# Kernel tuning notes

Hardware: AMD Instinct MI355X
Metric: run time of the kernel (lower is better)

Reference implementation:

```python
import jax, jax.numpy as jnp
import numpy as np

# Model hyperparameters (from init_kwargs)
D_MODEL, D_STATE, D_CONV, EXPAND, NHEADS, NGROUPS = 1024, 16, 4, 2, 8, 1
D_INNER = D_MODEL * EXPAND                      # 2048
HEADDIM = D_INNER // NHEADS                     # 256
D_XBC = D_INNER + 2 * NGROUPS * D_STATE         # conv channels: x + B + C
D_IN_PROJ = 3 * D_INNER + D_XBC + NHEADS        # z0 + x0 + z(unused) + xBC + dt
BATCH, SEQLEN = 2, 2048
LN_EPS = 1e-5


def setup_inputs() -> dict:
    key = jax.random.key(0)
    ks = jax.random.split(key, 8)
    u = jax.random.normal(ks[0], (BATCH, SEQLEN, D_MODEL), dtype=jnp.float32)
    W_in = jax.random.normal(ks[1], (D_IN_PROJ, D_MODEL), jnp.float32) / np.sqrt(D_MODEL)
    conv_w = jax.random.normal(ks[2], (D_XBC, 1, D_CONV), jnp.float32) / np.sqrt(D_CONV)
    conv_b = jnp.zeros((D_XBC,), jnp.float32)
    # dt_bias = inverse-softplus of dt ~ LogUniform(1e-3, 1e-1), as in source init
    dt = jnp.exp(jax.random.uniform(ks[3], (NHEADS,)) * (np.log(0.1) - np.log(0.001)) + np.log(0.001))
    dt_bias = dt + jnp.log(-jnp.expm1(-dt))
    A_log = jnp.log(jax.random.uniform(ks[4], (NHEADS,), minval=0.9, maxval=0.999))
    D_param = jnp.ones((NHEADS,), jnp.float32)
    ln_gamma = jnp.ones((D_INNER,), jnp.float32)
    ln_beta = jnp.zeros((D_INNER,), jnp.float32)
    W_gate = jax.random.normal(ks[5], (D_INNER, D_INNER), jnp.float32) / np.sqrt(D_INNER)
    b_gate = jnp.zeros((D_INNER,), jnp.float32)
    W_out = jax.random.normal(ks[6], (D_MODEL, 2 * D_INNER), jnp.float32) / np.sqrt(2 * D_INNER)
    return dict(u=u, W_in=W_in, conv_w=conv_w, conv_b=conv_b, dt_bias=dt_bias,
                A_log=A_log, D_param=D_param, ln_gamma=ln_gamma, ln_beta=ln_beta,
                W_gate=W_gate, b_gate=b_gate, W_out=W_out)


def _silu(x):
    return x * jax.nn.sigmoid(x)


def reference(u, W_in, conv_w, conv_b, dt_bias, A_log, D_param,
              ln_gamma, ln_beta, W_gate, b_gate, W_out):
    B, L, _ = u.shape
    zxbcdt = u @ W_in.T                                   # [B,L,D_IN_PROJ]
    z0 = zxbcdt[..., :D_INNER]
    x0 = zxbcdt[..., D_INNER:2 * D_INNER]
    # z = zxbcdt[..., 2*D_INNER:3*D_INNER]  # split but never used in source forward
    xBC = zxbcdt[..., 3 * D_INNER:3 * D_INNER + D_XBC]
    dt = jax.nn.softplus(zxbcdt[..., -NHEADS:] + dt_bias)  # [B,L,H]
    A = -jnp.exp(A_log)                                    # [H], per-head scalar

    # causal depthwise conv1d over time (left pad d_conv-1, crop to L)
    xBC_c = jnp.transpose(xBC, (0, 2, 1))                  # [B,C,L]
    xBC_c = jax.lax.conv_general_dilated(
        xBC_c, conv_w, window_strides=(1,), padding=[(D_CONV - 1, 0)],
        dimension_numbers=('NCH', 'OIH', 'NCH'), feature_group_count=D_XBC)
    xBC = _silu(jnp.transpose(xBC_c, (0, 2, 1)) + conv_b)  # [B,L,C]

    x = xBC[..., :D_INNER].reshape(B, L, NHEADS, HEADDIM)  # [B,L,H,P]
    Bm = xBC[..., D_INNER:D_INNER + D_STATE]               # [B,L,N] (ngroups=1)
    Cm = xBC[..., D_INNER + D_STATE:]                      # [B,L,N]

    def step(h, inp):
        x_t, B_t, C_t, dt_t = inp                          # [B,H,P],[B,N],[B,N],[B,H]
        dA = jnp.exp(dt_t * A)[:, :, None, None]           # [B,H,1,1]
        h = dA * h + (dt_t[:, :, None, None] * x_t[..., None]) * B_t[:, None, None, :]
        y_t = jnp.einsum('bhpn,bn->bhp', h, C_t) + D_param[None, :, None] * x_t
        return h, y_t

    h0 = jnp.zeros((B, NHEADS, HEADDIM, D_STATE), u.dtype)
    xs = (jnp.moveaxis(x, 1, 0), jnp.moveaxis(Bm, 1, 0),
          jnp.moveaxis(Cm, 1, 0), jnp.moveaxis(dt, 1, 0))
    _, y = jax.lax.scan(step, h0, xs)                      # [L,B,H,P]
    y = jnp.moveaxis(y, 0, 1).reshape(B, L, D_INNER)

    # LayerNorm
    mu = y.mean(-1, keepdims=True)
    var = ((y - mu) ** 2).mean(-1, keepdims=True)
    y = (y - mu) * jax.lax.rsqrt(var + LN_EPS) * ln_gamma + ln_beta

    gate = jax.nn.sigmoid(y @ W_gate.T + b_gate)
    y = gate * y

    mlp_skip = _silu(z0) * x0
    return jnp.concatenate([mlp_skip, y], axis=-1) @ W_out.T  # [B,L,D_MODEL]
```

## Files before the change

kernel.cpp:

```cpp
#include <hip/hip_runtime.h>
#include <hip/hip_bf16.h>
#include <math.h>

#define BATCH   2
#define SEQLEN  2048
#define DMODEL  1024
#define DINNER  2048
#define DSTATE  16
#define NHEADS  8
#define HEADDIM 256
#define DXBC    2080
#define NPACK   6184
#define NPAD    6400
#define MROWS   4096
#define CHUNK   64
#define NCHUNK  32
#define BH      16

typedef unsigned int u32;
typedef unsigned short u16;
typedef __attribute__((ext_vector_type(8))) short short8;
typedef __attribute__((ext_vector_type(4))) float f32x4;

#define GLOAD16(g, l) __builtin_amdgcn_global_load_lds( \
    (const __attribute__((address_space(1))) u32*)(g),  \
    (__attribute__((address_space(3))) u32*)(l), 16, 0, 0)

#define MFMA_B16(d, a, b) d = __builtin_amdgcn_mfma_f32_16x16x32_bf16(a, b, d, 0, 0, 0)

__device__ __forceinline__ u16 f2bf(float f) {
  union { float f; u32 u; } v; v.f = f;
  u32 r = v.u + 0x7fff + ((v.u >> 16) & 1);
  return (u16)(r >> 16);
}
__device__ __forceinline__ float bf2f(u16 b) {
  union { u32 u; float f; } v; v.u = ((u32)b) << 16;
  return v.f;
}

struct GParts { float* p0; float* p1; };

#define S_U   1048576
#define S_WG  1048576
#define S_WO  1048576
#define S_WP  1638400
#define S_TOT (S_U + S_WG + S_WO + S_WP)

__global__ void cvt_all(const float* __restrict__ u, const float* __restrict__ Wg,
                        const float* __restrict__ Wo, const float* __restrict__ Win,
                        u16* __restrict__ ub, u16* __restrict__ Wgb,
                        u16* __restrict__ Wob, u16* __restrict__ Wp) {
  for (int i = blockIdx.x * 256 + threadIdx.x; i < S_TOT; i += gridDim.x * 256) {
    const float* src; u16* dst; int idx;
    if (i < S_U) { src = u; dst = ub; idx = i; }
    else if (i < S_U + S_WG) { src = Wg; dst = Wgb; idx = i - S_U; }
    else if (i < S_U + S_WG + S_WO) { src = Wo; dst = Wob; idx = i - S_U - S_WG; }
    else {
      int j = i - S_U - S_WG - S_WO;
      int row = j >> 8, c4 = j & 255;
      ushort4 o = make_ushort4(0, 0, 0, 0);
      if (row < NPACK) {
        int orig = row < 4096 ? row : row + 2048;
        float4 v = ((const float4*)(Win + (size_t)orig * DMODEL))[c4];
        o = make_ushort4(f2bf(v.x), f2bf(v.y), f2bf(v.z), f2bf(v.w));
      }
      ((ushort4*)Wp)[j] = o;
      continue;
    }
    float4 v = ((const float4*)src)[idx];
    ((ushort4*)dst)[idx] = make_ushort4(f2bf(v.x), f2bf(v.y), f2bf(v.z), f2bf(v.w));
  }
}

template <int NL>
__device__ __forceinline__ void stage_rows(const u16* __restrict__ gsrc, int ldk,
                                           char* ldsmat, int row0, int w, int l) {
  const int rl = w * 8 + (l >> 3);
  const int q = ((l & 7) ^ (l >> 3)) * 8;
  #pragma unroll
  for (int j = 0; j < NL; ++j) {
    GLOAD16(gsrc + (size_t)(row0 + j * 64 + rl) * ldk + q,
            ldsmat + (row0 + j * 64 + w * 8) * 128);
  }
}

__device__ __forceinline__ short8 frag8(const char* mat, int row, int q) {
  return *(const short8*)(mat + row * 128 + ((q ^ (row & 7)) << 4));
}

__global__ __launch_bounds__(512, 1) void gemmA(
    const u16* __restrict__ A, const u16* __restrict__ B, int K, int ldk,
    int ldo, u16* __restrict__ outp) {
  __shared__ char lds[131072];
  const int tid = threadIdx.x;
  const int w = tid >> 6, l = tid & 63;
  const int wm = w >> 2, wn = w & 3;
  const int fr = l & 15, g = l >> 4;
  int s = blockIdx.y * gridDim.x + blockIdx.x;
  const int nwg = gridDim.x * gridDim.y;
  s = (s & 7) * (nwg >> 3) + (s >> 3);
  const int bx = s % gridDim.x, by = s / gridDim.x;
  const u16* Ap = A + (size_t)bx * 256 * ldk;
  const u16* Bp = B + (size_t)by * 256 * ldk;
  const int NT = K >> 6;

  f32x4 acc[8][4];
  #pragma unroll
  for (int m = 0; m < 8; ++m)
    #pragma unroll
    for (int n = 0; n < 4; ++n) acc[m][n] = (f32x4){0.f, 0.f, 0.f, 0.f};

  stage_rows<2>(Bp, ldk, lds + 32768, 0, w, l);
  stage_rows<2>(Bp, ldk, lds + 32768, 128, w, l);
  stage_rows<1>(Ap, ldk, lds, 0, w, l);
  stage_rows<1>(Ap, ldk, lds, 128, w, l);
  stage_rows<1>(Ap, ldk, lds, 64, w, l);
  stage_rows<1>(Ap, ldk, lds, 192, w, l);

  for (int t = 0; t < NT; ++t) {
    const bool last = (t == NT - 1);
    const char* cbA = lds + (t & 1) * 65536;
    const char* cbB = cbA + 32768;
    char* nbA = lds + ((t + 1) & 1) * 65536;
    char* nbB = nbA + 32768;
    const u16* An = Ap + (size_t)(t + 1) * 64;
    const u16* Bn = Bp + (size_t)(t + 1) * 64;

    asm volatile("s_waitcnt vmcnt(2)" ::: "memory");
    __builtin_amdgcn_s_barrier();
    __builtin_amdgcn_sched_barrier(0);

    short8 bf0[4], bf1[4];
    #pragma unroll
    for (int n = 0; n < 4; ++n) {
      bf0[n] = frag8(cbB, wn * 64 + n * 16 + fr, g);
      bf1[n] = frag8(cbB, wn * 64 + n * 16 + fr, 4 + g);
    }
    {
      short8 a00 = frag8(cbA, wm * 128 + fr, g);
      short8 a01 = frag8(cbA, wm * 128 + fr, 4 + g);
      short8 a10 = frag8(cbA, wm * 128 + 16 + fr, g);
      short8 a11 = frag8(cbA, wm * 128 + 16 + fr, 4 + g);
      if (!last) stage_rows<2>(Bn, ldk, nbB, 0, w, l);
      __builtin_amdgcn_sched_barrier(0);
      __builtin_amdgcn_s_setprio(1);
      #pragma unroll
      for (int n = 0; n < 4; ++n) { MFMA_B16(acc[0][n], a00, bf0[n]); MFMA_B16(acc[1][n], a10, bf0[n]); }
      #pragma unroll
      for (int n = 0; n < 4; ++n) { MFMA_B16(acc[0][n], a01, bf1[n]); MFMA_B16(acc[1][n], a11, bf1[n]); }
      __builtin_amdgcn_s_setprio(0);
    }
    {
      short8 a00 = frag8(cbA, wm * 128 + 32 + fr, g);
      short8 a01 = frag8(cbA, wm * 128 + 32 + fr, 4 + g);
      short8 a10 = frag8(cbA, wm * 128 + 48 + fr, g);
      short8 a11 = frag8(cbA, wm * 128 + 48 + fr, 4 + g);
      if (!last) stage_rows<2>(Bn, ldk, nbB, 128, w, l);
      __builtin_amdgcn_sched_barrier(0);
      __builtin_amdgcn_s_setprio(1);
      #pragma unroll
      for (int n = 0; n < 4; ++n) { MFMA_B16(acc[2][n], a00, bf0[n]); MFMA_B16(acc[3][n], a10, bf0[n]); }
      #pragma unroll
      for (int n = 0; n < 4; ++n) { MFMA_B16(acc[2][n], a01, bf1[n]); MFMA_B16(acc[3][n], a11, bf1[n]); }
      __builtin_amdgcn_s_setprio(0);
    }
    if (last) { asm volatile("s_waitcnt vmcnt(0)" ::: "memory"); }
    else      { asm volatile("s_waitcnt vmcnt(4)" ::: "memory"); }
    __builtin_amdgcn_s_barrier();
    __builtin_amdgcn_sched_barrier(0);
    {
      short8 a00 = frag8(cbA, wm * 128 + 64 + fr, g);
      short8 a01 = frag8(cbA, wm * 128 + 64 + fr, 4 + g);
      short8 a10 = frag8(cbA, wm * 128 + 80 + fr, g);
      short8 a11 = frag8(cbA, wm * 128 + 80 + fr, 4 + g);
      if (!last) { stage_rows<1>(An, ldk, nbA, 0, w, l); stage_rows<1>(An, ldk, nbA, 128, w, l); }
      __builtin_amdgcn_sched_barrier(0);
      __builtin_amdgcn_s_setprio(1);
      #pragma unroll
      for (int n = 0; n < 4; ++n) { MFMA_B16(acc[4][n], a00, bf0[n]); MFMA_B16(acc[5][n], a10, bf0[n]); }
      #pragma unroll
      for (int n = 0; n < 4; ++n) { MFMA_B16(acc[4][n], a01, bf1[n]); MFMA_B16(acc[5][n], a11, bf1[n]); }
      __builtin_amdgcn_s_setprio(0);
    }
    {
      short8 a00 = frag8(cbA, wm * 128 + 96 + fr, g);
      short8 a01 = frag8(cbA, wm * 128 + 96 + fr, 4 + g);
      short8 a10 = frag8(cbA, wm * 128 + 112 + fr, g);
      short8 a11 = frag8(cbA, wm * 128 + 112 + fr, 4 + g);
      if (!last) { stage_rows<1>(An, ldk, nbA, 64, w, l); stage_rows<1>(An, ldk, nbA, 192, w, l); }
      __builtin_amdgcn_sched_barrier(0);
      __builtin_amdgcn_s_setprio(1);
      #pragma unroll
      for (int n = 0; n < 4; ++n) { MFMA_B16(acc[6][n], a00, bf0[n]); MFMA_B16(acc[7][n], a10, bf0[n]); }
      #pragma unroll
      for (int n = 0; n < 4; ++n) { MFMA_B16(acc[6][n], a01, bf1[n]); MFMA_B16(acc[7][n], a11, bf1[n]); }
      __builtin_amdgcn_s_setprio(0);
    }
  }

  const int er = g * 4;
  #pragma unroll
  for (int m = 0; m < 8; ++m)
    #pragma unroll
    for (int n = 0; n < 4; ++n)
      #pragma unroll
      for (int j = 0; j < 4; ++j) {
        int row = bx * 256 + wm * 128 + m * 16 + er + j;
        int col = by * 256 + wn * 64 + n * 16 + fr;
        outp[(size_t)row * ldo + col] = f2bf(acc[m][n][j]);
      }
}

template <int EPI, int MAP>
__global__ __launch_bounds__(512, 1) void gemmB(
    const u16* __restrict__ A, const u16* __restrict__ B, int K_loop, int ldk,
    int ldo, void* __restrict__ outp, const float* __restrict__ bias,
    const u16* __restrict__ gate_in, GParts gp) {
  __shared__ char lds[3 * 49152];
  const int tid = threadIdx.x;
  const int w = tid >> 6, l = tid & 63;
  const int wm = w >> 1, wn = w & 1;
  const int fr = l & 15, g = l >> 4;
  int bx, by;
  if (MAP == 1) {
    int b = blockIdx.y * gridDim.x + blockIdx.x;
    int r = b >> 3;
    bx = 2 * (b & 7) + (r >> 4);
    by = r & 15;
  } else {
    int s = blockIdx.y * gridDim.x + blockIdx.x;
    const int nwg = gridDim.x * gridDim.y;
    s = (s & 7) * (nwg >> 3) + (s >> 3);
    bx = s % gridDim.x; by = s / gridDim.x;
  }
  const u16* Ap = A + (size_t)bx * 256 * ldk + (size_t)blockIdx.z * K_loop;
  const u16* Bp = B + (size_t)by * 128 * ldk + (size_t)blockIdx.z * K_loop;
  const int NT = K_loop >> 6;

  f32x4 acc[4][4];
  #pragma unroll
  for (int m = 0; m < 4; ++m)
    #pragma unroll
    for (int n = 0; n < 4; ++n) acc[m][n] = (f32x4){0.f, 0.f, 0.f, 0.f};

  #pragma unroll
  for (int p = 0; p < 2; ++p) {
    char* bA = lds + p * 49152;
    char* bB = bA + 32768;
    const u16* Ak = Ap + (size_t)p * 64;
    const u16* Bk = Bp + (size_t)p * 64;
    stage_rows<1>(Bk, ldk, bB, 0, w, l);
    stage_rows<1>(Bk, ldk, bB, 64, w, l);
    stage_rows<1>(Ak, ldk, bA, 0, w, l);
    stage_rows<1>(Ak, ldk, bA, 64, w, l);
    stage_rows<1>(Ak, ldk, bA, 128, w, l);
    stage_rows<1>(Ak, ldk, bA, 192, w, l);
  }

  int cur = 0;
  for (int t = 0; t < NT; ++t) {
    const bool last = (t == NT - 1);
    const bool dostage = (t + 2 < NT);
    int st = cur + 2; if (st >= 3) st -= 3;
    const char* cbA = lds + cur * 49152;
    const char* cbB = cbA + 32768;
    char* nbA = lds + st * 49152;
    char* nbB = nbA + 32768;
    const u16* An = Ap + (size_t)(t + 2) * 64;
    const u16* Bn = Bp + (size_t)(t + 2) * 64;

    if (last) { asm volatile("s_waitcnt vmcnt(0)" ::: "memory"); }
    else      { asm volatile("s_waitcnt vmcnt(6)" ::: "memory"); }
    __builtin_amdgcn_s_barrier();
    __builtin_amdgcn_sched_barrier(0);

    short8 bf0[4], bf1[4];
    #pragma unroll
    for (int n = 0; n < 4; ++n) {
      bf0[n] = frag8(cbB, wn * 64 + n * 16 + fr, g);
      bf1[n] = frag8(cbB, wn * 64 + n * 16 + fr, 4 + g);
    }
    {
      short8 a00 = frag8(cbA, wm * 64 + fr, g);
      short8 a01 = frag8(cbA, wm * 64 + fr, 4 + g);
      short8 a10 = frag8(cbA, wm * 64 + 16 + fr, g);
      short8 a11 = frag8(cbA, wm * 64 + 16 + fr, 4 + g);
      if (dostage) {
        stage_rows<1>(Bn, ldk, nbB, 0, w, l);
        stage_rows<1>(Bn, ldk, nbB, 64, w, l);
        stage_rows<1>(An, ldk, nbA, 0, w, l);
      }
      __builtin_amdgcn_sched_barrier(0);
      __builtin_amdgcn_s_setprio(1);
      #pragma unroll
      for (int n = 0; n < 4; ++n) { MFMA_B16(acc[0][n], a00, bf0[n]); MFMA_B16(acc[1][n], a10, bf0[n]); }
      #pragma unroll
      for (int n = 0; n < 4; ++n) { MFMA_B16(acc[0][n], a01, bf1[n]); MFMA_B16(acc[1][n], a11, bf1[n]); }
      __builtin_amdgcn_s_setprio(0);
    }
    {
      short8 a00 = frag8(cbA, wm * 64 + 32 + fr, g);
      short8 a01 = frag8(cbA, wm * 64 + 32 + fr, 4 + g);
      short8 a10 = frag8(cbA, wm * 64 + 48 + fr, g);
      short8 a11 = frag8(cbA, wm * 64 + 48 + fr, 4 + g);
      if (dostage) {
        stage_rows<1>(An, ldk, nbA, 64, w, l);
        stage_rows<1>(An, ldk, nbA, 128, w, l);
        stage_rows<1>(An, ldk, nbA, 192, w, l);
      }
      __builtin_amdgcn_sched_barrier(0);
      __builtin_amdgcn_s_setprio(1);
      #pragma unroll
      for (int n = 0; n < 4; ++n) { MFMA_B16(acc[2][n], a00, bf0[n]); MFMA_B16(acc[3][n], a10, bf0[n]); }
      #pragma unroll
      for (int n = 0; n < 4; ++n) { MFMA_B16(acc[2][n], a01, bf1[n]); MFMA_B16(acc[3][n], a11, bf1[n]); }
      __builtin_amdgcn_s_setprio(0);
    }
    cur = cur + 1; if (cur >= 3) cur = 0;
  }

  const int er = g * 4;
  float* pp = nullptr;
  if (EPI == 2) pp = blockIdx.z == 0 ? gp.p0 : gp.p1;
  #pragma unroll
  for (int m = 0; m < 4; ++m)
    #pragma unroll
    for (int n = 0; n < 4; ++n)
      #pragma unroll
      for (int j = 0; j < 4; ++j) {
        int row = bx * 256 + wm * 64 + m * 16 + er + j;
        int col = by * 128 + wn * 64 + n * 16 + fr;
        float v = acc[m][n][j];
        if (EPI == 1) {
          float gt = 1.f / (1.f + __expf(-(v + bias[col])));
          float nv = bf2f(gate_in[(size_t)row * 2048 + col]);
          ((u16*)outp)[(size_t)row * 4096 + 2048 + col] = f2bf(gt * nv);
        } else {
          pp[(size_t)row * ldo + col] = v;
        }
      }
}

__global__ void reduce2(const float* __restrict__ p0, const float* __restrict__ p1,
                        float* __restrict__ out) {
  const int n4 = MROWS * DMODEL / 4;
  for (int i = blockIdx.x * 256 + threadIdx.x; i < n4; i += gridDim.x * 256) {
    float4 a = ((const float4*)p0)[i];
    float4 b = ((const float4*)p1)[i];
    float4 o;
    o.x = a.x + b.x; o.y = a.y + b.y; o.z = a.z + b.z; o.w = a.w + b.w;
    ((float4*)out)[i] = o;
  }
}

#define NB_CONV 16640
#define NB_MLP  8192
#define NB_DT   128

__global__ void prep_kernel(const u16* __restrict__ zx, const float* __restrict__ cw,
                            const float* __restrict__ cb, u16* __restrict__ xc,
                            float* __restrict__ bc, u16* __restrict__ hcat,
                            const float* __restrict__ dt_bias, float* __restrict__ dtb) {
  int blk = blockIdx.x;
  if (blk < NB_CONV) {
    int idx = blk * 256 + threadIdx.x;
    int c2 = idx % (DXBC / 2);
    int m = idx / (DXBC / 2);
    int c = c2 * 2;
    int l = m & (SEQLEN - 1);
    const u16* col = zx + (size_t)m * NPAD + 4096 + c;
    float2 cbv = *(const float2*)(cb + c);
    float4 w0 = ((const float4*)cw)[c2 * 2];
    float4 w1 = ((const float4*)cw)[c2 * 2 + 1];
    float a0 = cbv.x, a1 = cbv.y;
    ushort2 t0 = *(const ushort2*)col;
    a0 += w0.w * bf2f(t0.x); a1 += w1.w * bf2f(t0.y);
    if (l >= 1) { ushort2 t = *(const ushort2*)(col - NPAD);     a0 += w0.z * bf2f(t.x); a1 += w1.z * bf2f(t.y); }
    if (l >= 2) { ushort2 t = *(const ushort2*)(col - 2 * NPAD); a0 += w0.y * bf2f(t.x); a1 += w1.y * bf2f(t.y); }
    if (l >= 3) { ushort2 t = *(const ushort2*)(col - 3 * NPAD); a0 += w0.x * bf2f(t.x); a1 += w1.x * bf2f(t.y); }
    float s0 = a0 / (1.f + __expf(-a0));
    float s1 = a1 / (1.f + __expf(-a1));
    if (c < DINNER) {
      ushort2 o; o.x = f2bf(s0); o.y = f2bf(s1);
      *(ushort2*)(xc + (size_t)m * DINNER + c) = o;
    } else {
      float2 o; o.x = s0; o.y = s1;
      *(float2*)(bc + (size_t)m * 32 + (c - DINNER)) = o;
    }
  } else if (blk < NB_CONV + NB_MLP) {
    int i = (blk - NB_CONV) * 256 + threadIdx.x;
    int m = i >> 9, c4 = (i & 511) * 4;
    const u16* row = zx + (size_t)m * NPAD;
    ushort4 zv = *(const ushort4*)(row + c4);
    ushort4 xv = *(const ushort4*)(row + 2048 + c4);
    float z0, x0;
    ushort4 o;
    z0 = bf2f(zv.x); x0 = bf2f(xv.x); o.x = f2bf(x0 * z0 / (1.f + __expf(-z0)));
    z0 = bf2f(zv.y); x0 = bf2f(xv.y); o.y = f2bf(x0 * z0 / (1.f + __expf(-z0)));
    z0 = bf2f(zv.z); x0 = bf2f(xv.z); o.z = f2bf(x0 * z0 / (1.f + __expf(-z0)));
    z0 = bf2f(zv.w); x0 = bf2f(xv.w); o.w = f2bf(x0 * z0 / (1.f + __expf(-z0)));
    *(ushort4*)(hcat + (size_t)m * 4096 + c4) = o;
  } else {
    int idx = (blk - NB_CONV - NB_MLP) * 256 + threadIdx.x;
    if (idx >= MROWS * NHEADS) return;
    int hd = idx & 7, m = idx >> 3;
    float raw = bf2f(zx[(size_t)m * NPAD + 6176 + hd]) + dt_bias[hd];
    float dtv = raw > 20.f ? raw : log1pf(expf(raw));
    dtb[idx] = dtv;
  }
}

__device__ __forceinline__ int xs_addr(int r, int p) {
  return r * 512 + ((((p >> 3) ^ ((r >> 3) & 3)) & 31) << 4) + (p & 7) * 2;
}
__device__ __forceinline__ int P_addr(int t, int s) {
  return t * 128 + ((((s >> 3) ^ (t & 7)) & 7) << 4) + (s & 7) * 2;
}

__device__ __forceinline__ void stage_x(u16* xs, const u16* __restrict__ xc,
                                        size_t base, int tid) {
  #pragma unroll
  for (int it = 0; it < 8; ++it) {
    int r = it * 8 + (tid >> 5);
    int pc = (tid & 31) * 8;
    short8 v = *(const short8*)(xc + base + (size_t)r * DINNER + pc);
    *(short8*)((char*)xs + xs_addr(r, pc)) = v;
  }
}

__device__ __forceinline__ short8 xfrag(const u16* xs, int k0, int g, int p) {
  short8 v;
  #pragma unroll
  for (int j = 0; j < 8; ++j) {
    int s = k0 + g * 8 + j;
    v[j] = *(const short*)((const char*)xs + xs_addr(s, p));
  }
  return v;
}

__global__ __launch_bounds__(256) void ssd_state(
    const u16* __restrict__ xc, const float* __restrict__ bcb,
    const float* __restrict__ dtb, const float* __restrict__ A_log,
    float* __restrict__ Sbuf, float* __restrict__ lcbuf) {
  __shared__ u16 xs[64 * 256];
  __shared__ float sLC[64], sDT[64];
  __shared__ float wBT[16][65];
  const int tid = threadIdx.x;
  const int bh = blockIdx.x >> 5, c = blockIdx.x & 31;
  const int b = bh >> 3, h = bh & 7;
  const size_t row0 = (size_t)b * SEQLEN + c * CHUNK;
  stage_x(xs, xc, row0 * DINNER + h * HEADDIM, tid);
  if (tid < 64) {
    float dtv = dtb[(row0 + tid) * NHEADS + h];
    float A = -__expf(A_log[h]);
    float s = dtv * A;
    #pragma unroll
    for (int off = 1; off < 64; off <<= 1) {
      float v = __shfl_up(s, off, 64);
      if (tid >= off) s += v;
    }
    sLC[tid] = s; sDT[tid] = dtv;
    lcbuf[(size_t)blockIdx.x * 64 + tid] = s;
  }
  __syncthreads();
  const float lc63 = sLC[63];
  for (int i = tid; i < 1024; i += 256) {
    int n = i & 15, t = i >> 4;
    float w = sDT[t] * __expf(lc63 - sLC[t]);
    wBT[n][t] = w * bcb[(row0 + t) * 32 + n];
  }
  __syncthreads();
  const int lane = tid & 63, w = tid >> 6;
  const int cl = lane & 15, g = lane >> 4;
  f32x4 acc[4];
  #pragma unroll
  for (int pt = 0; pt < 4; ++pt) acc[pt] = (f32x4){0.f, 0.f, 0.f, 0.f};
  #pragma unroll
  for (int kk = 0; kk < 2; ++kk) {
    int k0 = kk * 32;
    short8 af;
    #pragma unroll
    for (int j = 0; j < 8; ++j) af[j] = (short)f2bf(wBT[cl][k0 + g * 8 + j]);
    #pragma unroll
    for (int pt = 0; pt < 4; ++pt) {
      short8 bf = xfrag(xs, k0, g, (w * 4 + pt) * 16 + cl);
      acc[pt] = __builtin_amdgcn_mfma_f32_16x16x32_bf16(af, bf, acc[pt], 0, 0, 0);
    }
  }
  float* Sc = Sbuf + (size_t)blockIdx.x * 16 * 256;
  #pragma unroll
  for (int pt = 0; pt < 4; ++pt)
    #pragma unroll
    for (int j = 0; j < 4; ++j)
      Sc[(g * 4 + j) * 256 + (w * 4 + pt) * 16 + cl] = acc[pt][j];
}

__global__ __launch_bounds__(256) void ssd_combine(
    const float* __restrict__ Sbuf, const float* __restrict__ lcbuf,
    float* __restrict__ Sprev) {
  const int bh = blockIdx.x >> 4, seg = blockIdx.x & 15;
  const int idx = seg * 256 + threadIdx.x;
  float r = 0.f;
  #pragma unroll 1
  for (int c = 0; c < NCHUNK; ++c) {
    size_t o = ((size_t)bh * NCHUNK + c) * 4096 + idx;
    Sprev[o] = r;
    float lam = __expf(lcbuf[((size_t)bh * NCHUNK + c) * 64 + 63]);
    r = lam * r + Sbuf[o];
  }
}

__global__ __launch_bounds__(256) void ssd_out(
    const u16* __restrict__ xc, const float* __restrict__ bcb,
    const float* __restrict__ dtb, const float* __restrict__ lcbuf,
    const float* __restrict__ Sprev, const float* __restrict__ D_par,
    u16* __restrict__ y) {
  __shared__ u16 xs[64 * 256];
  __shared__ u16 P[64 * 64];
  __shared__ u16 sB[64][17], sC[64][17], sCe[64][17];
  __shared__ u16 sSp[256][17];
  __shared__ float sLC[64], sDT[64];
  const int tid = threadIdx.x;
  const int bh = blockIdx.x >> 5, c = blockIdx.x & 31;
  const int b = bh >> 3, h = bh & 7;
  const size_t row0 = (size_t)b * SEQLEN + c * CHUNK;
  stage_x(xs, xc, row0 * DINNER + h * HEADDIM, tid);
  if (tid < 64) {
    sLC[tid] = lcbuf[(size_t)blockIdx.x * 64 + tid];
    sDT[tid] = dtb[(row0 + tid) * NHEADS + h];
  }
  for (int i = tid; i < 1024; i += 256) {
    int n = i & 15, t = i >> 4;
    float Bv = bcb[(row0 + t) * 32 + n];
    float Cv = bcb[(row0 + t) * 32 + 16 + n];
    float e = __expf(lcbuf[(size_t)blockIdx.x * 64 + t]);
    sB[t][n] = f2bf(Bv);
    sC[t][n] = f2bf(Cv);
    sCe[t][n] = f2bf(Cv * e);
  }
  {
    const float* Sp = Sprev + (size_t)blockIdx.x * 4096;
    int p = tid & 255;
    if (tid < 256) {
      #pragma unroll
      for (int n = 0; n < 16; ++n) sSp[p][n] = f2bf(Sp[n * 256 + p]);
    }
  }
  __syncthreads();

  const int lane = tid & 63, w = tid >> 6;
  const int cl = lane & 15, g = lane >> 4;

  f32x4 gacc[4];
  #pragma unroll
  for (int st = 0; st < 4; ++st) gacc[st] = (f32x4){0.f, 0.f, 0.f, 0.f};
  short8 afc = (short8){0, 0, 0, 0, 0, 0, 0, 0};
  if (g < 2) {
    #pragma unroll
    for (int j = 0; j < 8; ++j) afc[j] = (short)sC[w * 16 + cl][g * 8 + j];
  }
  #pragma unroll
  for (int st = 0; st < 4; ++st) {
    short8 bfb = (short8){0, 0, 0, 0, 0, 0, 0, 0};
    if (g < 2) {
      #pragma unroll
      for (int j = 0; j < 8; ++j) bfb[j] = (short)sB[st * 16 + cl][g * 8 + j];
    }
    gacc[st] = __builtin_amdgcn_mfma_f32_16x16x32_bf16(afc, bfb, gacc[st], 0, 0, 0);
  }
  #pragma unroll
  for (int st = 0; st < 4; ++st) {
    #pragma unroll
    for (int j = 0; j < 4; ++j) {
      int t = w * 16 + g * 4 + j;
      int s = st * 16 + cl;
      float v = 0.f;
      if (s <= t) v = gacc[st][j] * sDT[s] * __expf(sLC[t] - sLC[s]);
      *(u16*)((char*)P + P_addr(t, s)) = f2bf(v);
    }
  }
  asm volatile("s_waitcnt lgkmcnt(0)" ::: "memory");
  __builtin_amdgcn_sched_barrier(0);

  f32x4 acc[16];
  #pragma unroll
  for (int pt = 0; pt < 16; ++pt) acc[pt] = (f32x4){0.f, 0.f, 0.f, 0.f};
  #pragma unroll
  for (int kk = 0; kk < 2; ++kk) {
    int k0 = kk * 32;
    short8 ap = *(const short8*)((const char*)P + P_addr(w * 16 + cl, k0 + g * 8));
    #pragma unroll
    for (int pt = 0; pt < 16; ++pt) {
      short8 bf = xfrag(xs, k0, g, pt * 16 + cl);
      acc[pt] = __builtin_amdgcn_mfma_f32_16x16x32_bf16(ap, bf, acc[pt], 0, 0, 0);
    }
  }
  {
    short8 ae = (short8){0, 0, 0, 0, 0, 0, 0, 0};
    if (g < 2) {
      #pragma unroll
      for (int j = 0; j < 8; ++j) ae[j] = (short)sCe[w * 16 + cl][g * 8 + j];
    }
    #pragma unroll
    for (int pt = 0; pt < 16; ++pt) {
      short8 bs = (short8){0, 0, 0, 0, 0, 0, 0, 0};
      if (g < 2) {
        #pragma unroll
        for (int j = 0; j < 8; ++j) bs[j] = (short)sSp[pt * 16 + cl][g * 8 + j];
      }
      acc[pt] = __builtin_amdgcn_mfma_f32_16x16x32_bf16(ae, bs, acc[pt], 0, 0, 0);
    }
  }
  const float Dv = D_par[h];
  #pragma unroll
  for (int pt = 0; pt < 16; ++pt) {
    #pragma unroll
    for (int j = 0; j < 4; ++j) {
      int t = w * 16 + g * 4 + j;
      int p = pt * 16 + cl;
      float xv = bf2f(*(const u16*)((const char*)xs + xs_addr(t, p)));
      float v = acc[pt][j] + Dv * xv;
      y[(row0 + t) * DINNER + h * HEADDIM + p] = f2bf(v);
    }
  }
}

__global__ __launch_bounds__(256) void ln_kernel(const u16* __restrict__ y,
                                                 const float* __restrict__ gamma,
                                                 const float* __restrict__ beta,
                                                 u16* __restrict__ nrm) {
  const int row = blockIdx.x;
  const int t = threadIdx.x;
  const u16* yr = y + (size_t)row * DINNER;
  short8 v = *(const short8*)(yr + t * 8);
  float f[8];
  float s = 0.f, ss = 0.f;
  #pragma unroll
  for (int j = 0; j < 8; ++j) {
    f[j] = bf2f((u16)v[j]);
    s += f[j]; ss += f[j] * f[j];
  }
  #pragma unroll
  for (int o = 1; o < 64; o <<= 1) { s += __shfl_xor(s, o); ss += __shfl_xor(ss, o); }
  __shared__ float rs[4], rss[4];
  const int wid = t >> 6;
  if ((t & 63) == 0) { rs[wid] = s; rss[wid] = ss; }
  __syncthreads();
  s = rs[0] + rs[1] + rs[2] + rs[3];
  ss = rss[0] + rss[1] + rss[2] + rss[3];
  float mu = s * (1.f / DINNER);
  float var = ss * (1.f / DINNER) - mu * mu;
  float inv = rsqrtf(var + 1e-5f);
  float4 g0 = ((const float4*)gamma)[t * 2], g1 = ((const float4*)gamma)[t * 2 + 1];
  float4 b0 = ((const float4*)beta)[t * 2], b1 = ((const float4*)beta)[t * 2 + 1];
  short8 o;
  o[0] = (short)f2bf((f[0] - mu) * inv * g0.x + b0.x);
  o[1] = (short)f2bf((f[1] - mu) * inv * g0.y + b0.y);
  o[2] = (short)f2bf((f[2] - mu) * inv * g0.z + b0.z);
  o[3] = (short)f2bf((f[3] - mu) * inv * g0.w + b0.w);
  o[4] = (short)f2bf((f[4] - mu) * inv * g1.x + b1.x);
  o[5] = (short)f2bf((f[5] - mu) * inv * g1.y + b1.y);
  o[6] = (short)f2bf((f[6] - mu) * inv * g1.z + b1.z);
  o[7] = (short)f2bf((f[7] - mu) * inv * g1.w + b1.w);
  *(short8*)(nrm + (size_t)row * DINNER + t * 8) = o;
}

extern "C" void kernel_launch(void* const* d_in, const int* in_sizes, int n_in,
                              void* d_out, int out_size, void* d_ws, size_t ws_size,
                              hipStream_t stream) {
  (void)in_sizes; (void)n_in; (void)out_size; (void)ws_size;
  const float* u       = (const float*)d_in[0];
  const float* W_in    = (const float*)d_in[1];
  const float* conv_w  = (const float*)d_in[2];
  const float* conv_b  = (const float*)d_in[3];
  const float* dt_bias = (const float*)d_in[4];
  const float* A_log   = (const float*)d_in[5];
  const float* D_par   = (const float*)d_in[6];
  const float* ln_g    = (const float*)d_in[7];
  const float* ln_b    = (const float*)d_in[8];
  const float* W_gate  = (const float*)d_in[9];
  const float* b_gate  = (const float*)d_in[10];
  const float* W_out   = (const float*)d_in[11];
  float* out = (float*)d_out;

  size_t off = 0;
  auto take = [&](size_t bytes) -> char* {
    char* p = (char*)d_ws + off;
    off = (off + bytes + 255) & ~(size_t)255;
    return p;
  };
  u16* u16b  = (u16*)take((size_t)MROWS * DMODEL * 2);
  u16* Wp    = (u16*)take((size_t)NPAD * DMODEL * 2);
  u16* Wg    = (u16*)take((size_t)DINNER * DINNER * 2);
  u16* Wo    = (u16*)take((size_t)DMODEL * 2 * DINNER * 2);
  u16* zx    = (u16*)take((size_t)MROWS * NPAD * 2);
  u16* xc    = (u16*)take((size_t)MROWS * DINNER * 2);
  float* bcb = (float*)take((size_t)MROWS * 32 * 4);
  float* dtb = (float*)take((size_t)MROWS * NHEADS * 4);
  float* lcbuf = (float*)take((size_t)BH * NCHUNK * 64 * 4);
  u16* nrm   = (u16*)take((size_t)MROWS * DINNER * 2);
  u16* hcat  = (u16*)take((size_t)MROWS * 2 * DINNER * 2);

  float* Sbuf  = (float*)u16b;
  u16*   y     = zx;
  float* Sprev = (float*)((char*)zx + (size_t)16 * 1024 * 1024);
  GParts parts2;
  parts2.p0 = (float*)zx;
  parts2.p1 = (float*)((char*)zx + (size_t)16 * 1024 * 1024);
  GParts none = {nullptr, nullptr};

  cvt_all<<<4096, 256, 0, stream>>>(u, W_gate, W_out, W_in, u16b, Wg, Wo, Wp);

  gemmA<<<dim3(MROWS / 256, NPAD / 256), 512, 0, stream>>>(
      u16b, Wp, DMODEL, DMODEL, NPAD, zx);

  prep_kernel<<<NB_CONV + NB_MLP + NB_DT, 256, 0, stream>>>(
      zx, conv_w, conv_b, xc, bcb, hcat, dt_bias, dtb);

  ssd_state<<<BH * NCHUNK, 256, 0, stream>>>(xc, bcb, dtb, A_log, Sbuf, lcbuf);
  ssd_combine<<<BH * 16, 256, 0, stream>>>(Sbuf, lcbuf, Sprev);
  ssd_out<<<BH * NCHUNK, 256, 0, stream>>>(xc, bcb, dtb, lcbuf, Sprev, D_par, y);

  ln_kernel<<<MROWS, 256, 0, stream>>>(y, ln_g, ln_b, nrm);

  gemmB<1, 1><<<dim3(MROWS / 256, DINNER / 128), 512, 0, stream>>>(
      nrm, Wg, DINNER, DINNER, 0, hcat, b_gate, nrm, none);

  gemmB<2, 0><<<dim3(MROWS / 256, DMODEL / 128, 2), 512, 0, stream>>>(
      hcat, Wo, 2 * DINNER / 2, 2 * DINNER, DMODEL, nullptr, nullptr, nullptr, parts2);

  reduce2<<<2048, 256, 0, stream>>>(parts2.p0, parts2.p1, out);
}
```

Baseline: 247.6 us.

## Replace 256x128 triple-buffered GEMM with 128x128 double-buffered two-block-per-CU kernel

The gate and output-projection GEMMs now use 128x128 tiles, 256 threads, double-buffered LDS of 64KB and launch bounds allowing two blocks per CU, replacing the 256x128, 512-thread, triple-buffered kernel. All A/B fragments for a k-step are loaded up front, a second barrier protects buffer reuse before issuing the next stage, and a new XCD-aware block mapping groups row tiles per XCD. The intent is better occupancy and more blocks to fill the CUs. The cost is lower per-block reuse, an extra barrier per iteration and shallower prefetch depth.

```diff
diff --git a/kernel.cpp b/kernel.cpp
--- a/kernel.cpp
+++ b/kernel.cpp
@@ -84,6 +84,18 @@
   }
 }
 
+template <int NG>
+__device__ __forceinline__ void stage_rows4(const u16* __restrict__ gsrc, int ldk,
+                                            char* ldsmat, int w, int l) {
+  const int rl = w * 8 + (l >> 3);
+  const int q = ((l & 7) ^ (l >> 3)) * 8;
+  #pragma unroll
+  for (int j = 0; j < NG; ++j) {
+    GLOAD16(gsrc + (size_t)(j * 32 + rl) * ldk + q,
+            ldsmat + (j * 32 + w * 8) * 128);
+  }
+}
+
 __device__ __forceinline__ short8 frag8(const char* mat, int row, int q) {
   return *(const short8*)(mat + row * 128 + ((q ^ (row & 7)) << 4));
 }
@@ -212,28 +224,28 @@
 }
 
 template <int EPI, int MAP>
-__global__ __launch_bounds__(512, 1) void gemmB(
+__global__ __launch_bounds__(256, 2) void gemm128(
     const u16* __restrict__ A, const u16* __restrict__ B, int K_loop, int ldk,
     int ldo, void* __restrict__ outp, const float* __restrict__ bias,
     const u16* __restrict__ gate_in, GParts gp) {
-  __shared__ char lds[3 * 49152];
+  __shared__ char lds[65536];
   const int tid = threadIdx.x;
   const int w = tid >> 6, l = tid & 63;
   const int wm = w >> 1, wn = w & 1;
   const int fr = l & 15, g = l >> 4;
   int bx, by;
-  if (MAP == 1) {
+  if (MAP == 2) {
     int b = blockIdx.y * gridDim.x + blockIdx.x;
-    int r = b >> 3;
-    bx = 2 * (b & 7) + (r >> 4);
-    by = r & 15;
+    int xcd = b & 7, local = b >> 3;
+    bx = 4 * xcd + (local & 3);
+    by = local >> 2;
   } else {
     int s = blockIdx.y * gridDim.x + blockIdx.x;
     const int nwg = gridDim.x * gridDim.y;
     s = (s & 7) * (nwg >> 3) + (s >> 3);
     bx = s % gridDim.x; by = s / gridDim.x;
   }
-  const u16* Ap = A + (size_t)bx * 256 * ldk + (size_t)blockIdx.z * K_loop;
+  const u16* Ap = A + (size_t)bx * 128 * ldk + (size_t)blockIdx.z * K_loop;
   const u16* Bp = B + (size_t)by * 128 * ldk + (size_t)blockIdx.z * K_loop;
   const int NT = K_loop >> 6;
 
@@ -243,80 +255,48 @@
     #pragma unroll
     for (int n = 0; n < 4; ++n) acc[m][n] = (f32x4){0.f, 0.f, 0.f, 0.f};
 
-  #pragma unroll
-  for (int p = 0; p < 2; ++p) {
-    char* bA = lds + p * 49152;
-    char* bB = bA + 32768;
-    const u16* Ak = Ap + (size_t)p * 64;
-    const u16* Bk = Bp + (size_t)p * 64;
-    stage_rows<1>(Bk, ldk, bB, 0, w, l);
-    stage_rows<1>(Bk, ldk, bB, 64, w, l);
-    stage_rows<1>(Ak, ldk, bA, 0, w, l);
-    stage_rows<1>(Ak, ldk, bA, 64, w, l);
-    stage_rows<1>(Ak, ldk, bA, 128, w, l);
-    stage_rows<1>(Ak, ldk, bA, 192, w, l);
-  }
-
-  int cur = 0;
+  stage_rows4<4>(Ap, ldk, lds, w, l);
+  stage_rows4<4>(Bp, ldk, lds + 16384, w, l);
+  stage_rows4<4>(Ap + 64, ldk, lds + 32768, w, l);
+  stage_rows4<4>(Bp + 64, ldk, lds + 49152, w, l);
+
   for (int t = 0; t < NT; ++t) {
-    const bool last = (t == NT - 1);
-    const bool dostage = (t + 2 < NT);
-    int st = cur + 2; if (st >= 3) st -= 3;
-    const char* cbA = lds + cur * 49152;
-    const char* cbB = cbA + 32768;
-    char* nbA = lds + st * 49152;
-    char* nbB = nbA + 32768;
-    const u16* An = Ap + (size_t)(t + 2) * 64;
-    const u16* Bn = Bp + (size_t)(t + 2) * 64;
-
-    if (last) { asm volatile("s_waitcnt vmcnt(0)" ::: "memory"); }
-    else      { asm volatile("s_waitcnt vmcnt(6)" ::: "memory"); }
+    if (t + 1 < NT) { asm volatile("s_waitcnt vmcnt(8)" ::: "memory"); }
+    else            { asm volatile("s_waitcnt vmcnt(0)" ::: "memory"); }
     __builtin_amdgcn_s_barrier();
     __builtin_amdgcn_sched_barrier(0);
 
-    short8 bf0[4], bf1[4];
+    const char* cbA = lds + (t & 1) * 32768;
+    const char* cbB = cbA + 16384;
+    short8 af[4][2], bfr[4][2];
+    #pragma unroll
+    for (int m = 0; m < 4; ++m) {
+      af[m][0] = frag8(cbA, wm * 64 + m * 16 + fr, g);
+      af[m][1] = frag8(cbA, wm * 64 + m * 16 + fr, 4 + g);
+    }
     #pragma unroll
     for (int n = 0; n < 4; ++n) {
-      bf0[n] = frag8(cbB, wn * 64 + n * 16 + fr, g);
-      bf1[n] = frag8(cbB, wn * 64 + n * 16 + fr, 4 + g);
-    }
-    {
-      short8 a00 = frag8(cbA, wm * 64 + fr, g);
-      short8 a01 = frag8(cbA, wm * 64 + fr, 4 + g);
-      short8 a10 = frag8(cbA, wm * 64 + 16 + fr, g);
-      short8 a11 = frag8(cbA, wm * 64 + 16 + fr, 4 + g);
-      if (dostage) {
-        stage_rows<1>(Bn, ldk, nbB, 0, w, l);
-        stage_rows<1>(Bn, ldk, nbB, 64, w, l);
-        stage_rows<1>(An, ldk, nbA, 0, w, l);
+      bfr[n][0] = frag8(cbB, wn * 64 + n * 16 + fr, g);
+      bfr[n][1] = frag8(cbB, wn * 64 + n * 16 + fr, 4 + g);
+    }
+    asm volatile("s_waitcnt lgkmcnt(0)" ::: "memory");
+    __builtin_amdgcn_s_barrier();
+    __builtin_amdgcn_sched_barrier(0);
+    if (t + 2 < NT) {
+      char* nb = lds + (t & 1) * 32768;
+      stage_rows4<4>(Ap + (size_t)(t + 2) * 64, ldk, nb, w, l);
+      stage_rows4<4>(Bp + (size_t)(t + 2) * 64, ldk, nb + 16384, w, l);
+    }
+    __builtin_amdgcn_sched_barrier(0);
+    __builtin_amdgcn_s_setprio(1);
+    #pragma unroll
+    for (int m = 0; m < 4; ++m)
+      #pragma unroll
+      for (int n = 0; n < 4; ++n) {
+        MFMA_B16(acc[m][n], af[m][0], bfr[n][0]);
+        MFMA_B16(acc[m][n], af[m][1], bfr[n][1]);
       }
-      __builtin_amdgcn_sched_barrier(0);
-      __builtin_amdgcn_s_setprio(1);
-      #pragma unroll
-      for (int n = 0; n < 4; ++n) { MFMA_B16(acc[0][n], a00, bf0[n]); MFMA_B16(acc[1][n], a10, bf0[n]); }
-      #pragma unroll
-      for (int n = 0; n < 4; ++n) { MFMA_B16(acc[0][n], a01, bf1[n]); MFMA_B16(acc[1][n], a11, bf1[n]); }
-      __builtin_amdgcn_s_setprio(0);
-    }
-    {
-      short8 a00 = frag8(cbA, wm * 64 + 32 + fr, g);
-      short8 a01 = frag8(cbA, wm * 64 + 32 + fr, 4 + g);
-      short8 a10 = frag8(cbA, wm * 64 + 48 + fr, g);
-      short8 a11 = frag8(cbA, wm * 64 + 48 + fr, 4 + g);
-      if (dostage) {
-        stage_rows<1>(An, ldk, nbA, 64, w, l);
-        stage_rows<1>(An, ldk, nbA, 128, w, l);
-        stage_rows<1>(An, ldk, nbA, 192, w, l);
-      }
-      __builtin_amdgcn_sched_barrier(0);
-      __builtin_amdgcn_s_setprio(1);
-      #pragma unroll
-      for (int n = 0; n < 4; ++n) { MFMA_B16(acc[2][n], a00, bf0[n]); MFMA_B16(acc[3][n], a10, bf0[n]); }
-      #pragma unroll
-      for (int n = 0; n < 4; ++n) { MFMA_B16(acc[2][n], a01, bf1[n]); MFMA_B16(acc[3][n], a11, bf1[n]); }
-      __builtin_amdgcn_s_setprio(0);
-    }
-    cur = cur + 1; if (cur >= 3) cur = 0;
+    __builtin_amdgcn_s_setprio(0);
   }
 
   const int er = g * 4;
@@ -328,7 +308,7 @@
     for (int n = 0; n < 4; ++n)
       #pragma unroll
       for (int j = 0; j < 4; ++j) {
-        int row = bx * 256 + wm * 64 + m * 16 + er + j;
+        int row = bx * 128 + wm * 64 + m * 16 + er + j;
         int col = by * 128 + wn * 64 + n * 16 + fr;
         float v = acc[m][n][j];
         if (EPI == 1) {
@@ -723,10 +703,10 @@
 
   ln_kernel<<<MROWS, 256, 0, stream>>>(y, ln_g, ln_b, nrm);
 
-  gemmB<1, 1><<<dim3(MROWS / 256, DINNER / 128), 512, 0, stream>>>(
+  gemm128<1, 2><<<dim3(MROWS / 128, DINNER / 128), 256, 0, stream>>>(
       nrm, Wg, DINNER, DINNER, 0, hcat, b_gate, nrm, none);
 
-  gemmB<2, 0><<<dim3(MROWS / 256, DMODEL / 128, 2), 512, 0, stream>>>(
+  gemm128<2, 0><<<dim3(MROWS / 128, DMODEL / 128, 2), 256, 0, stream>>>(
       hcat, Wo, 2 * DINNER / 2, 2 * DINNER, DMODEL, nullptr, nullptr, nullptr, parts2);
 
   reduce2<<<2048, 256, 0, stream>>>(parts2.p0, parts2.p1, out);
```

Measured after the change: 254.7 us. 1.03x slower.

## Fuse SiLU-gated MLP skip into in-projection GEMM epilogue via interleaved weights

Applied to the files above, without the earlier changes.

Interleaves z0 and x0 rows of the packed in-projection weight so that adjacent output columns hold a z/x pair. The GEMM epilogue then combines them with a lane shuffle and writes silu(z)*x straight into hcat. The separate MLP-skip pass in the prep kernel and the large zx intermediate go away, and only the xBC/dt columns are stored into a narrower buffer. Buffer aliasing is rearranged so Sprev and the partial outputs reuse the weight and xc regions, which relies on those buffers being dead by the time they are overwritten.

```diff
diff --git a/kernel.cpp b/kernel.cpp
--- a/kernel.cpp
+++ b/kernel.cpp
@@ -12,6 +12,7 @@
 #define DXBC    2080
 #define NPACK   6184
 #define NPAD    6400
+#define NPADX   2304
 #define MROWS   4096
 #define CHUNK   64
 #define NCHUNK  32
@@ -60,7 +61,7 @@
       int row = j >> 8, c4 = j & 255;
       ushort4 o = make_ushort4(0, 0, 0, 0);
       if (row < NPACK) {
-        int orig = row < 4096 ? row : row + 2048;
+        int orig = row < 4096 ? (row >> 1) + ((row & 1) << 11) : row + 2048;
         float4 v = ((const float4*)(Win + (size_t)orig * DMODEL))[c4];
         o = make_ushort4(f2bf(v.x), f2bf(v.y), f2bf(v.z), f2bf(v.w));
       }
@@ -90,7 +91,7 @@
 
 __global__ __launch_bounds__(512, 1) void gemmA(
     const u16* __restrict__ A, const u16* __restrict__ B, int K, int ldk,
-    int ldo, u16* __restrict__ outp) {
+    u16* __restrict__ zx2, u16* __restrict__ hcat) {
   __shared__ char lds[131072];
   const int tid = threadIdx.x;
   const int w = tid >> 6, l = tid & 63;
@@ -207,7 +208,16 @@
       for (int j = 0; j < 4; ++j) {
         int row = bx * 256 + wm * 128 + m * 16 + er + j;
         int col = by * 256 + wn * 64 + n * 16 + fr;
-        outp[(size_t)row * ldo + col] = f2bf(acc[m][n][j]);
+        float v = acc[m][n][j];
+        if (by < 16) {
+          float p = __shfl_xor(v, 1);
+          if ((l & 1) == 0) {
+            float r = p * v / (1.f + __expf(-v));
+            hcat[(size_t)row * 4096 + (col >> 1)] = f2bf(r);
+          }
+        } else {
+          zx2[(size_t)row * NPADX + (col - 4096)] = f2bf(v);
+        }
       }
 }
 
@@ -354,12 +364,11 @@
 }
 
 #define NB_CONV 16640
-#define NB_MLP  8192
 #define NB_DT   128
 
-__global__ void prep_kernel(const u16* __restrict__ zx, const float* __restrict__ cw,
+__global__ void prep_kernel(const u16* __restrict__ zx2, const float* __restrict__ cw,
                             const float* __restrict__ cb, u16* __restrict__ xc,
-                            float* __restrict__ bc, u16* __restrict__ hcat,
+                            float* __restrict__ bc,
                             const float* __restrict__ dt_bias, float* __restrict__ dtb) {
   int blk = blockIdx.x;
   if (blk < NB_CONV) {
@@ -368,16 +377,16 @@
     int m = idx / (DXBC / 2);
     int c = c2 * 2;
     int l = m & (SEQLEN - 1);
-    const u16* col = zx + (size_t)m * NPAD + 4096 + c;
+    const u16* col = zx2 + (size_t)m * NPADX + c;
     float2 cbv = *(const float2*)(cb + c);
     float4 w0 = ((const float4*)cw)[c2 * 2];
     float4 w1 = ((const float4*)cw)[c2 * 2 + 1];
     float a0 = cbv.x, a1 = cbv.y;
     ushort2 t0 = *(const ushort2*)col;
     a0 += w0.w * bf2f(t0.x); a1 += w1.w * bf2f(t0.y);
-    if (l >= 1) { ushort2 t = *(const ushort2*)(col - NPAD);     a0 += w0.z * bf2f(t.x); a1 += w1.z * bf2f(t.y); }
-    if (l >= 2) { ushort2 t = *(const ushort2*)(col - 2 * NPAD); a0 += w0.y * bf2f(t.x); a1 += w1.y * bf2f(t.y); }
-    if (l >= 3) { ushort2 t = *(const ushort2*)(col - 3 * NPAD); a0 += w0.x * bf2f(t.x); a1 += w1.x * bf2f(t.y); }
+    if (l >= 1) { ushort2 t = *(const ushort2*)(col - NPADX);     a0 += w0.z * bf2f(t.x); a1 += w1.z * bf2f(t.y); }
+    if (l >= 2) { ushort2 t = *(const ushort2*)(col - 2 * NPADX); a0 += w0.y * bf2f(t.x); a1 += w1.y * bf2f(t.y); }
+    if (l >= 3) { ushort2 t = *(const ushort2*)(col - 3 * NPADX); a0 += w0.x * bf2f(t.x); a1 += w1.x * bf2f(t.y); }
     float s0 = a0 / (1.f + __expf(-a0));
     float s1 = a1 / (1.f + __expf(-a1));
     if (c < DINNER) {
@@ -387,24 +396,11 @@
       float2 o; o.x = s0; o.y = s1;
       *(float2*)(bc + (size_t)m * 32 + (c - DINNER)) = o;
     }
-  } else if (blk < NB_CONV + NB_MLP) {
-    int i = (blk - NB_CONV) * 256 + threadIdx.x;
-    int m = i >> 9, c4 = (i & 511) * 4;
-    const u16* row = zx + (size_t)m * NPAD;
-    ushort4 zv = *(const ushort4*)(row + c4);
-    ushort4 xv = *(const ushort4*)(row + 2048 + c4);
-    float z0, x0;
-    ushort4 o;
-    z0 = bf2f(zv.x); x0 = bf2f(xv.x); o.x = f2bf(x0 * z0 / (1.f + __expf(-z0)));
-    z0 = bf2f(zv.y); x0 = bf2f(xv.y); o.y = f2bf(x0 * z0 / (1.f + __expf(-z0)));
-    z0 = bf2f(zv.z); x0 = bf2f(xv.z); o.z = f2bf(x0 * z0 / (1.f + __expf(-z0)));
-    z0 = bf2f(zv.w); x0 = bf2f(xv.w); o.w = f2bf(x0 * z0 / (1.f + __expf(-z0)));
-    *(ushort4*)(hcat + (size_t)m * 4096 + c4) = o;
   } else {
-    int idx = (blk - NB_CONV - NB_MLP) * 256 + threadIdx.x;
+    int idx = (blk - NB_CONV) * 256 + threadIdx.x;
     if (idx >= MROWS * NHEADS) return;
     int hd = idx & 7, m = idx >> 3;
-    float raw = bf2f(zx[(size_t)m * NPAD + 6176 + hd]) + dt_bias[hd];
+    float raw = bf2f(zx2[(size_t)m * NPADX + 2080 + hd]) + dt_bias[hd];
     float dtv = raw > 20.f ? raw : log1pf(expf(raw));
     dtb[idx] = dtv;
   }
@@ -693,7 +689,7 @@
   u16* Wp    = (u16*)take((size_t)NPAD * DMODEL * 2);
   u16* Wg    = (u16*)take((size_t)DINNER * DINNER * 2);
   u16* Wo    = (u16*)take((size_t)DMODEL * 2 * DINNER * 2);
-  u16* zx    = (u16*)take((size_t)MROWS * NPAD * 2);
+  u16* zx2   = (u16*)take((size_t)MROWS * NPADX * 2);
   u16* xc    = (u16*)take((size_t)MROWS * DINNER * 2);
   float* bcb = (float*)take((size_t)MROWS * 32 * 4);
   float* dtb = (float*)take((size_t)MROWS * NHEADS * 4);
@@ -702,20 +698,20 @@
   u16* hcat  = (u16*)take((size_t)MROWS * 2 * DINNER * 2);
 
   float* Sbuf  = (float*)u16b;
-  u16*   y     = zx;
-  float* Sprev = (float*)((char*)zx + (size_t)16 * 1024 * 1024);
+  float* Sprev = (float*)Wp;
+  u16*   y     = zx2;
   GParts parts2;
-  parts2.p0 = (float*)zx;
-  parts2.p1 = (float*)((char*)zx + (size_t)16 * 1024 * 1024);
+  parts2.p0 = (float*)d_ws;
+  parts2.p1 = (float*)xc;
   GParts none = {nullptr, nullptr};
 
   cvt_all<<<4096, 256, 0, stream>>>(u, W_gate, W_out, W_in, u16b, Wg, Wo, Wp);
 
   gemmA<<<dim3(MROWS / 256, NPAD / 256), 512, 0, stream>>>(
-      u16b, Wp, DMODEL, DMODEL, NPAD, zx);
-
-  prep_kernel<<<NB_CONV + NB_MLP + NB_DT, 256, 0, stream>>>(
-      zx, conv_w, conv_b, xc, bcb, hcat, dt_bias, dtb);
+      u16b, Wp, DMODEL, DMODEL, zx2, hcat);
+
+  prep_kernel<<<NB_CONV + NB_DT, 256, 0, stream>>>(
+      zx2, conv_w, conv_b, xc, bcb, dt_bias, dtb);
 
   ssd_state<<<BH * NCHUNK, 256, 0, stream>>>(xc, bcb, dtb, A_log, Sbuf, lcbuf);
   ssd_combine<<<BH * 16, 256, 0, stream>>>(Sbuf, lcbuf, Sprev);
```

Result: slower. 270.7 us (+9.3%).
